# Optimization experiments

Measured on AMD Instinct MI355X. Metric: run time of the kernel, lower is better.

The kernel has to match this reference:

```python
import jax, jax.numpy as jnp
import numpy as np

REG = 0.05  # reg_param > 0 -> entropic (logsumexp) branch
N, M, D = 16384, 8192, 128


def setup_inputs() -> dict:
    key = jax.random.key(0)
    k1, k2, k3 = jax.random.split(key, 3)
    source_data = jax.random.normal(k1, (N, D), dtype=jnp.float32)
    target_data = jax.random.normal(k2, (M, D), dtype=jnp.float32)
    psi = jax.random.normal(k3, (M,), dtype=jnp.float32) * 0.1
    return {"source_data": source_data, "target_data": target_data, "psi": psi}


def reference(source_data, target_data, psi):
    # squared norms
    ty2 = jnp.sum(target_data ** 2, axis=1)            # [M]
    sx2 = jnp.sum(source_data ** 2, axis=1, keepdims=True)  # [N,1]
    scale = jnp.mean(ty2)                              # scalar normalizer
    # pairwise squared-distance cost, normalized (matches torch expansion)
    cost_xy = (sx2 + ty2[None, :] - 2.0 * source_data @ target_data.T) / scale  # [N,M]
    # entropic semi-dual: -reg * logsumexp((psi - c)/reg) averaged over x
    lse = jax.nn.logsumexp((psi[None, :] - cost_xy) / REG, axis=1)  # [N]
    cte = REG * jnp.log(jnp.asarray(M, dtype=jnp.float32))
    return jnp.mean(-REG * lse) + jnp.mean(psi) + cte
```

## Files before the change

kernel.cpp:

```cpp
#include <hip/hip_runtime.h>
#include <stdint.h>

#define REG_P   0.05f
#define LOG2E   1.4426950408889634f
#define LN2     0.6931471805599453f
#define NSPLIT  8

typedef int   int32x8 __attribute__((ext_vector_type(8)));
typedef float floatx4 __attribute__((ext_vector_type(4)));

__device__ inline int32x8 load32B(const void* p) {
    union { int32x8 v; uint4 q[2]; } u;
    u.q[0] = ((const uint4*)p)[0];
    u.q[1] = ((const uint4*)p)[1];
    return u.v;
}

__device__ inline float block_sum_f(const float* __restrict__ v, int M, int tid,
                                    float* redbuf) {
    float s = 0.f;
    const float4* v4 = (const float4*)v;
    for (int j = tid; j < (M >> 2); j += 256) {
        float4 q = v4[j];
        s += (q.x + q.y) + (q.z + q.w);
    }
    #pragma unroll
    for (int mask = 1; mask < 64; mask <<= 1) s += __shfl_xor(s, mask, 64);
    int wv = tid >> 6, lane = tid & 63;
    if (lane == 0) redbuf[wv] = s;
    __syncthreads();
    return (redbuf[0] + redbuf[1]) + (redbuf[2] + redbuf[3]);
}

__global__ void k1_pack(const float* __restrict__ src, const float* __restrict__ tgt,
                        unsigned char* __restrict__ Sb8, unsigned char* __restrict__ Tbs8,
                        float* __restrict__ sx2, float* __restrict__ ty2,
                        float* __restrict__ out, int N, int M) {
    int tid = threadIdx.x;
    if (blockIdx.x == 0 && tid == 0) out[0] = 0.0f;
    int r16 = tid >> 4;
    int c8  = tid & 15;
    int row_id = blockIdx.x * 16 + r16;
    bool isS = row_id < N;
    int row = isS ? row_id : row_id - N;
    const float4* sp = (const float4*)((isS ? src : tgt) + (size_t)row * 128 + c8 * 8);
    float4 f0 = sp[0], f1 = sp[1];
    int w0 = 0, w1 = 0;
    w0 = __builtin_amdgcn_cvt_pk_fp8_f32(f0.x, f0.y, w0, false);
    w0 = __builtin_amdgcn_cvt_pk_fp8_f32(f0.z, f0.w, w0, true);
    w1 = __builtin_amdgcn_cvt_pk_fp8_f32(f1.x, f1.y, w1, false);
    w1 = __builtin_amdgcn_cvt_pk_fp8_f32(f1.z, f1.w, w1, true);
    uint2 val = make_uint2((unsigned)w0, (unsigned)w1);
    float sq = f0.x*f0.x + f0.y*f0.y + f0.z*f0.z + f0.w*f0.w
             + f1.x*f1.x + f1.y*f1.y + f1.z*f1.z + f1.w*f1.w;
    #pragma unroll
    for (int mask = 1; mask < 16; mask <<= 1) sq += __shfl_xor(sq, mask, 16);
    if (isS) {
        ((uint2*)(Sb8 + (size_t)row * 128 + c8 * 8))[0] = val;
        if (c8 == 0) sx2[row] = sq;
    } else {
        int t = row >> 6, jc = row & 63;
        int ct = jc >> 4, l16 = jc & 15;
        int quad = c8 >> 2, rem = c8 & 3;
        size_t dst = (size_t)t * 8192 + (size_t)((ct * 64 + quad * 16 + l16) * 32 + rem * 8);
        ((uint2*)(Tbs8 + dst))[0] = val;
        if (c8 == 0) ty2[row] = sq;
    }
}

__global__ __launch_bounds__(256, 4) void k3_main(
    const unsigned char* __restrict__ Sb8, const unsigned char* __restrict__ Tbs8,
    const float* __restrict__ psi, const float* __restrict__ ty2,
    float* __restrict__ lpart, int N, int M) {
    __shared__ float sb2a[1024];
    __shared__ float redA[4];
    const int tid  = threadIdx.x;
    const int lane = tid & 63;
    const int wv   = tid >> 6;
    const int quad = lane >> 4, l16 = lane & 15;
    const int b = blockIdx.x;
    const int split = b & 7;
    const int i0 = (b >> 3) * 128;
    const int mspan = M / NSPLIT;
    const int jstart = split * mspan;

    float ty2sum = block_sum_f(ty2, M, tid, redA);
    float scale = ty2sum / (float)M;
    float c1 = 1.0f / (REG_P * scale);
    float a2 = 2.0f * LOG2E / (REG_P * scale);

    for (int idx = tid; idx < mspan; idx += 256) {
        int j = jstart + idx;
        sb2a[idx] = (psi[j] * (1.0f / REG_P) - ty2[j] * c1) * LOG2E;
    }
    __syncthreads();

    int32x8 afrag[2];
    #pragma unroll
    for (int rt = 0; rt < 2; ++rt)
        afrag[rt] = load32B(Sb8 + (size_t)(i0 + wv * 32 + rt * 16 + l16) * 128 + quad * 32);

    float ls[2][4];
    #pragma unroll
    for (int rt = 0; rt < 2; ++rt)
        #pragma unroll
        for (int r = 0; r < 4; ++r) ls[rt][r] = 0.0f;

    const unsigned char* gb = Tbs8 + (size_t)jstart * 128 + (size_t)lane * 32;
    const floatx4 zero4 = (floatx4){0.f, 0.f, 0.f, 0.f};
    const int SC = 0x7F7F7F7F;

    int32x8 bc = load32B(gb);
    int32x8 bn = load32B(gb + 2048);
    floatx4 pA, pB;
    float bvP = 0.0f;

    #pragma unroll 4
    for (int u = 0; u < 64; ++u) {
        float bv = sb2a[u * 16 + l16];
        floatx4 c0 = __builtin_amdgcn_mfma_scale_f32_16x16x128_f8f6f4(
            afrag[0], bc, zero4, 0, 0, 0, SC, 0, SC);
        floatx4 c1v = __builtin_amdgcn_mfma_scale_f32_16x16x128_f8f6f4(
            afrag[1], bc, zero4, 0, 0, 0, SC, 0, SC);
        int32x8 bf = load32B(gb + (size_t)(u + 2) * 2048);
        if (u) {
            #pragma unroll
            for (int r = 0; r < 4; ++r) {
                ls[0][r] += __builtin_amdgcn_exp2f(fmaf(a2, pA[r], bvP));
                ls[1][r] += __builtin_amdgcn_exp2f(fmaf(a2, pB[r], bvP));
            }
        }
        pA = c0; pB = c1v; bvP = bv;
        bc = bn; bn = bf;
    }
    #pragma unroll
    for (int r = 0; r < 4; ++r) {
        ls[0][r] += __builtin_amdgcn_exp2f(fmaf(a2, pA[r], bvP));
        ls[1][r] += __builtin_amdgcn_exp2f(fmaf(a2, pB[r], bvP));
    }

    #pragma unroll
    for (int rt = 0; rt < 2; ++rt)
        #pragma unroll
        for (int r = 0; r < 4; ++r) {
            float v = ls[rt][r];
            #pragma unroll
            for (int mask = 1; mask < 16; mask <<= 1) v += __shfl_xor(v, mask, 64);
            if (l16 == 0) {
                int rowg = i0 + wv * 32 + rt * 16 + quad * 4 + r;
                lpart[(size_t)rowg * NSPLIT + split] = v;
            }
        }
}

__global__ void k4_reduce(const float* __restrict__ lpart,
                          const float* __restrict__ sx2,
                          const float* __restrict__ psi,
                          const float* __restrict__ ty2,
                          float* __restrict__ out, int N, int M) {
    __shared__ float redA[4];
    __shared__ float redB[4];
    int tid = threadIdx.x;
    float ty2s = block_sum_f(ty2, M, tid, redA);
    float scale = ty2s / (float)M;

    int i = blockIdx.x * 256 + tid;
    const float4* lp = (const float4*)(lpart + (size_t)i * NSPLIT);
    float4 p0 = lp[0], p1 = lp[1];
    float s = (p0.x + p0.y + p0.z + p0.w) + (p1.x + p1.y + p1.z + p1.w);
    float L2 = __builtin_amdgcn_logf(s);
    float t = (-REG_P * LN2 * L2 + sx2[i] / scale) * (1.0f / (float)N);
    if (i < M) t += psi[i] * (1.0f / (float)M);
    #pragma unroll
    for (int mask = 1; mask < 64; mask <<= 1) t += __shfl_xor(t, mask, 64);
    int wv = tid >> 6, lane = tid & 63;
    if (lane == 0) redB[wv] = t;
    __syncthreads();
    if (tid == 0) {
        float total = (redB[0] + redB[1]) + (redB[2] + redB[3]);
        if (blockIdx.x == 0) total += REG_P * logf((float)M);
        atomicAdd(out, total);
    }
}

extern "C" void kernel_launch(void* const* d_in, const int* in_sizes, int n_in,
                              void* d_out, int out_size, void* d_ws, size_t ws_size,
                              hipStream_t stream) {
    const float* src = (const float*)d_in[0];
    const float* tgt = (const float*)d_in[1];
    const float* psi = (const float*)d_in[2];
    const int D = 128;
    const int N = in_sizes[0] / D;
    const int M = in_sizes[1] / D;

    char* ws = (char*)d_ws;
    float* sx2   = (float*)ws;
    float* ty2   = (float*)(ws + (size_t)N * 4);
    float* lpart = (float*)(ws + (size_t)N * 4 + (size_t)M * 4);
    size_t off = (size_t)N * 4 + (size_t)M * 4 + (size_t)N * NSPLIT * 4;
    off = (off + 255) & ~(size_t)255;
    unsigned char* Sb8  = (unsigned char*)(ws + off);
    unsigned char* Tbs8 = Sb8 + (size_t)N * 128;

    k1_pack<<<(N + M) / 16, 256, 0, stream>>>(src, tgt, Sb8, Tbs8, sx2, ty2,
                                              (float*)d_out, N, M);
    k3_main<<<(N / 128) * NSPLIT, 256, 0, stream>>>(Sb8, Tbs8, psi, ty2, lpart, N, M);
    k4_reduce<<<N / 256, 256, 0, stream>>>(lpart, sx2, psi, ty2, (float*)d_out, N, M);
}
```

Before: 96.94 us.

## Stage target fp8 tiles through double-buffered LDS shared across waves

Instead of every wave loading the same B fragments from global memory, the block cooperatively loads each 16 KB chunk of packed target data into a double-buffered LDS array. The next chunk is prefetched into registers while the current one is consumed by MFMAs. The A-fragment and first-chunk loads are also hoisted ahead of the ty2 reduction to hide their latency. This cuts the redundant global/L2 traffic (four waves fetching identical data) at the cost of 32 KB of LDS per block, which may lower occupancy below the 4 blocks per CU requested, and it adds a barrier per chunk.

```diff
diff --git a/kernel.cpp b/kernel.cpp
--- a/kernel.cpp
+++ b/kernel.cpp
@@ -74,6 +74,7 @@
     float* __restrict__ lpart, int N, int M) {
     __shared__ float sb2a[1024];
     __shared__ float redA[4];
+    __shared__ unsigned char bbuf[2][16384];
     const int tid  = threadIdx.x;
     const int lane = tid & 63;
     const int wv   = tid >> 6;
@@ -84,6 +85,20 @@
     const int mspan = M / NSPLIT;
     const int jstart = split * mspan;
 
+    const unsigned char* gsplit = Tbs8 + (size_t)jstart * 128;
+
+    uint4 st[4];
+    {
+        const uint4* gp = (const uint4*)gsplit;
+        #pragma unroll
+        for (int r = 0; r < 4; ++r) st[r] = gp[tid + r * 256];
+    }
+
+    int32x8 afrag[2];
+    #pragma unroll
+    for (int rt = 0; rt < 2; ++rt)
+        afrag[rt] = load32B(Sb8 + (size_t)(i0 + wv * 32 + rt * 16 + l16) * 128 + quad * 32);
+
     float ty2sum = block_sum_f(ty2, M, tid, redA);
     float scale = ty2sum / (float)M;
     float c1 = 1.0f / (REG_P * scale);
@@ -93,45 +108,57 @@
         int j = jstart + idx;
         sb2a[idx] = (psi[j] * (1.0f / REG_P) - ty2[j] * c1) * LOG2E;
     }
+
+    {
+        uint4* lp = (uint4*)&bbuf[0][0];
+        #pragma unroll
+        for (int r = 0; r < 4; ++r) lp[tid + r * 256] = st[r];
+    }
     __syncthreads();
 
-    int32x8 afrag[2];
+    float ls[2][4];
     #pragma unroll
     for (int rt = 0; rt < 2; ++rt)
-        afrag[rt] = load32B(Sb8 + (size_t)(i0 + wv * 32 + rt * 16 + l16) * 128 + quad * 32);
-
-    float ls[2][4];
-    #pragma unroll
-    for (int rt = 0; rt < 2; ++rt)
         #pragma unroll
         for (int r = 0; r < 4; ++r) ls[rt][r] = 0.0f;
 
-    const unsigned char* gb = Tbs8 + (size_t)jstart * 128 + (size_t)lane * 32;
     const floatx4 zero4 = (floatx4){0.f, 0.f, 0.f, 0.f};
     const int SC = 0x7F7F7F7F;
 
-    int32x8 bc = load32B(gb);
-    int32x8 bn = load32B(gb + 2048);
     floatx4 pA, pB;
     float bvP = 0.0f;
 
-    #pragma unroll 4
-    for (int u = 0; u < 64; ++u) {
-        float bv = sb2a[u * 16 + l16];
-        floatx4 c0 = __builtin_amdgcn_mfma_scale_f32_16x16x128_f8f6f4(
-            afrag[0], bc, zero4, 0, 0, 0, SC, 0, SC);
-        floatx4 c1v = __builtin_amdgcn_mfma_scale_f32_16x16x128_f8f6f4(
-            afrag[1], bc, zero4, 0, 0, 0, SC, 0, SC);
-        int32x8 bf = load32B(gb + (size_t)(u + 2) * 2048);
-        if (u) {
+    for (int g = 0; g < 8; ++g) {
+        if (g < 7) {
+            const uint4* gp = (const uint4*)(gsplit + (size_t)(g + 1) * 16384);
             #pragma unroll
-            for (int r = 0; r < 4; ++r) {
-                ls[0][r] += __builtin_amdgcn_exp2f(fmaf(a2, pA[r], bvP));
-                ls[1][r] += __builtin_amdgcn_exp2f(fmaf(a2, pB[r], bvP));
+            for (int r = 0; r < 4; ++r) st[r] = gp[tid + r * 256];
+        }
+        const unsigned char* lbase = &bbuf[g & 1][0] + (size_t)lane * 32;
+        #pragma unroll
+        for (int u = 0; u < 8; ++u) {
+            int uu = g * 8 + u;
+            float bv = sb2a[uu * 16 + l16];
+            int32x8 bc = load32B(lbase + u * 2048);
+            floatx4 c0 = __builtin_amdgcn_mfma_scale_f32_16x16x128_f8f6f4(
+                afrag[0], bc, zero4, 0, 0, 0, SC, 0, SC);
+            floatx4 c1v = __builtin_amdgcn_mfma_scale_f32_16x16x128_f8f6f4(
+                afrag[1], bc, zero4, 0, 0, 0, SC, 0, SC);
+            if (uu != 0) {
+                #pragma unroll
+                for (int r = 0; r < 4; ++r) {
+                    ls[0][r] += __builtin_amdgcn_exp2f(fmaf(a2, pA[r], bvP));
+                    ls[1][r] += __builtin_amdgcn_exp2f(fmaf(a2, pB[r], bvP));
+                }
             }
-        }
-        pA = c0; pB = c1v; bvP = bv;
-        bc = bn; bn = bf;
+            pA = c0; pB = c1v; bvP = bv;
+        }
+        if (g < 7) {
+            uint4* lp = (uint4*)&bbuf[(g + 1) & 1][0];
+            #pragma unroll
+            for (int r = 0; r < 4; ++r) lp[tid + r * 256] = st[r];
+            __syncthreads();
+        }
     }
     #pragma unroll
     for (int r = 0; r < 4; ++r) {
```

Result: slower. 120.3 us (+24.1%).
